# Optimization experiments

Hardware: AMD Instinct MI355X
Metric: run time of the kernel (lower is better)

Reference implementation:

```python
import jax, jax.numpy as jnp
import numpy as np

N = 50000
D_IN = 256
OUT = 16
HEADS = 32
GAT_C = OUT  # out_channels + beta_on(=0)


def _gat_conv(x, src, dst, W, att_src, att_dst, bias):
    """PyG GATConv, concat=False (mean over heads), with self-loops already appended."""
    n = x.shape[0]
    xp = (x @ W).reshape(n, HEADS, GAT_C)            # [N,H,C]
    a_s = jnp.einsum('nhc,hc->nh', xp, att_src)       # [N,H]
    a_d = jnp.einsum('nhc,hc->nh', xp, att_dst)       # [N,H]
    e = jax.nn.leaky_relu(a_s[src] + a_d[dst], 0.2)   # [E,H]
    # segment softmax over incoming edges of each dst node
    m = jax.ops.segment_max(e, dst, num_segments=n)
    e = jnp.exp(e - m[dst])
    s = jax.ops.segment_sum(e, dst, num_segments=n)
    alpha = e / (s[dst] + 1e-16)                      # [E,H]
    out = jax.ops.segment_sum(alpha[:, :, None] * xp[src], dst, num_segments=n)  # [N,H,C]
    return out.mean(axis=1) + bias                    # [N,C]


def setup_inputs() -> dict:
    key = jax.random.key(0)
    ks = jax.random.split(key, 16)
    E = 800000
    x = jax.random.normal(ks[0], (N, D_IN), dtype=jnp.float32)
    edge_index = jax.random.randint(ks[1], (2, E), 0, N, dtype=jnp.int64)
    sc = 1.0 / np.sqrt(D_IN)
    W1 = jax.random.normal(ks[2], (D_IN, HEADS * GAT_C), dtype=jnp.float32) * sc
    att_src1 = jax.random.normal(ks[3], (HEADS, GAT_C), dtype=jnp.float32) * 0.1
    att_dst1 = jax.random.normal(ks[4], (HEADS, GAT_C), dtype=jnp.float32) * 0.1
    b1 = jnp.zeros((GAT_C,), dtype=jnp.float32)
    W2 = jax.random.normal(ks[5], (D_IN, HEADS * GAT_C), dtype=jnp.float32) * sc
    att_src2 = jax.random.normal(ks[6], (HEADS, GAT_C), dtype=jnp.float32) * 0.1
    att_dst2 = jax.random.normal(ks[7], (HEADS, GAT_C), dtype=jnp.float32) * 0.1
    b2 = jnp.zeros((GAT_C,), dtype=jnp.float32)
    lin1_w = jax.random.normal(ks[8], (D_IN, 4 * OUT), dtype=jnp.float32) * sc
    lin1_b = jnp.zeros((4 * OUT,), dtype=jnp.float32)
    lin2_w = jax.random.normal(ks[9], (4 * OUT, OUT), dtype=jnp.float32) * (1.0 / np.sqrt(4 * OUT))
    lin2_b = jnp.zeros((OUT,), dtype=jnp.float32)
    return {"x": x, "edge_index": edge_index,
            "W1": W1, "att_src1": att_src1, "att_dst1": att_dst1, "b1": b1,
            "W2": W2, "att_src2": att_src2, "att_dst2": att_dst2, "b2": b2,
            "lin1_w": lin1_w, "lin1_b": lin1_b, "lin2_w": lin2_w, "lin2_b": lin2_b}


def reference(x, edge_index, W1, att_src1, att_dst1, b1, W2, att_src2, att_dst2, b2,
              lin1_w, lin1_b, lin2_w, lin2_b):
    n = x.shape[0]
    loops = jnp.arange(n, dtype=edge_index.dtype)
    # conv1: flow source_to_target on edge_index -> aggregate src=row0 into dst=row1
    src = jnp.concatenate([edge_index[0], loops])
    dst = jnp.concatenate([edge_index[1], loops])
    x_in = jax.nn.elu(_gat_conv(x, src, dst, W1, att_src1, att_dst1, b1))
    # conv2: flow target_to_source on transposed edge_index -> same effective (src,dst)
    x_out = jax.nn.elu(_gat_conv(x, src, dst, W2, att_src2, att_dst2, b2))
    x1 = jax.nn.elu(x @ lin1_w + lin1_b)
    x_self = jax.nn.elu(x1 @ lin2_w + lin2_b)
    return (x_in, x_out, x_self)
```

## Files before the change

kernel.cpp:

```cpp
#include <hip/hip_runtime.h>

typedef __bf16 bf16x8 __attribute__((ext_vector_type(8)));
typedef float  f32x4  __attribute__((ext_vector_type(4)));
typedef float  f32x2  __attribute__((ext_vector_type(2)));

#define NNODES   50000
#define DIN      256
#define HEADS    32
#define CDIM     16
#define NH       512
#define ERAW     800000
#define ZB       196
#define LDSW     280
#define LOG2E    1.4426950408889634f
#define CAST_B   12500
#define PREP_B   (CAST_B + ZB + 18)
#define GEMM_T   782
#define GEMMG    (2 * GEMM_T)
#define SCAT_B   3125
#define MLP_B    196
#define MIX1_B   (2 * SCAT_B + 3 + MLP_B)
#define MIX2_B   (2 * GEMMG + MLP_B)
#define DEGCAP   64

#if __has_builtin(__builtin_amdgcn_exp2f)
#define EXP2(x) __builtin_amdgcn_exp2f(x)
#else
#define EXP2(x) __expf((x) * 0.6931471805599453f)
#endif

__device__ __forceinline__ float b2f(unsigned short u) {
    return __uint_as_float(((unsigned)u) << 16);
}
__device__ __forceinline__ unsigned short f2b(float f) {
    unsigned v = __float_as_uint(f);
    v += 0x7fffu + ((v >> 16) & 1u);
    return (unsigned short)(v >> 16);
}

__global__ void __launch_bounds__(256) k_prep(
        const float* __restrict__ x, unsigned short* __restrict__ xb,
        const float* __restrict__ W0, const float* __restrict__ W1,
        const float* __restrict__ w1, const float* __restrict__ w2,
        unsigned short* __restrict__ Wt2, unsigned short* __restrict__ w1t,
        unsigned short* __restrict__ w2t,
        const int* __restrict__ ei, int* __restrict__ flag,
        int* __restrict__ cur) {
    __shared__ unsigned short T[64][258];
    int bid = blockIdx.x, t = threadIdx.x;

    if (bid < CAST_B) {
        int i = bid * 256 + t;
        float4 v = *(const float4*)(x + (size_t)i * 4);
        ushort4 o;
        o.x = f2b(v.x); o.y = f2b(v.y); o.z = f2b(v.z); o.w = f2b(v.w);
        *(ushort4*)(xb + (size_t)i * 4) = o;
        return;
    }
    if (bid < CAST_B + ZB) {
        int i = (bid - CAST_B) * 256 + t;
        if (i < NNODES) cur[i] = 0;
        if (bid == CAST_B && t == 0) {
            int nz = 0;
            #pragma unroll
            for (int k = 0; k < 64; ++k) nz |= ei[2 * k + 1];
            flag[0] = (nz == 0) ? 1 : 0;
        }
        return;
    }
    int tb = bid - (CAST_B + ZB);
    if (tb == 17) {
        for (int idx = t; idx < 1024; idx += 256) {
            int n = idx >> 6, k = idx & 63;
            w2t[n * 64 + k] = f2b(w2[k * CDIM + n]);
        }
        return;
    }
    const float* src; unsigned short* dst; int srcStride, doPi, tile;
    if (tb < 8)       { src = W0; dst = Wt2;             srcStride = NH; doPi = 1; tile = tb; }
    else if (tb < 16) { src = W1; dst = Wt2 + 512 * DIN; srcStride = NH; doPi = 1; tile = tb - 8; }
    else              { src = w1; dst = w1t;             srcStride = 64; doPi = 0; tile = 0; }
    int n0 = tile * 64;
    int nl = (t & 15) * 4;
    int kr = t >> 4;
    for (int kk = 0; kk < 256; kk += 16) {
        int k = kk + kr;
        float4 v = *(const float4*)(src + (size_t)k * srcStride + n0 + nl);
        T[nl + 0][k] = f2b(v.x);
        T[nl + 1][k] = f2b(v.y);
        T[nl + 2][k] = f2b(v.z);
        T[nl + 3][k] = f2b(v.w);
    }
    __syncthreads();
    int rl = t >> 2;
    int pr = doPi ? (((rl & 15) << 2) | (rl >> 4)) : rl;
    #pragma unroll
    for (int j = 0; j < 16; ++j) {
        int c4 = (t & 3) + 4 * j;
        ushort2 o0 = *(const ushort2*)&T[pr][c4 * 4];
        ushort2 o1 = *(const ushort2*)&T[pr][c4 * 4 + 2];
        ushort4 o; o.x = o0.x; o.y = o0.y; o.z = o1.x; o.w = o1.y;
        *(ushort4*)(dst + ((size_t)(n0 + rl)) * DIN + c4 * 4) = o;
    }
}

__device__ __forceinline__ void scat_body(int bid, int t,
        const int* __restrict__ ei, const int* __restrict__ flag,
        int* __restrict__ cur, int* __restrict__ csr) {
    int e = bid * 256 + t;
    int s, d;
    if (flag[0]) { s = ei[2 * e]; d = ei[2 * ERAW + 2 * e]; }
    else         { s = ei[e];     d = ei[ERAW + e]; }
    int pos = atomicAdd(&cur[d], 1);
    if (pos < DEGCAP) csr[(d << 6) + pos] = s;
}

__device__ __forceinline__ void gemm_body(int bid, int tid,
        const unsigned short* __restrict__ xb,
        const unsigned short* __restrict__ Wt,
        unsigned* __restrict__ xp8,
        const float* __restrict__ att_src, const float* __restrict__ att_dst,
        float* __restrict__ a_s, float* __restrict__ a_d,
        unsigned short* As) {
    int row0 = (bid >> 1) * 64;
    int ch   = bid & 1;
    int w = tid >> 6, lane = tid & 63;
    int r = lane & 15, quad = lane >> 4;

    {
        int row = tid >> 2, slot = tid & 3;
        const uint4* g = (const uint4*)(xb + (size_t)(row0 + row) * DIN);
        uint4* l = (uint4*)(As + row * LDSW);
        #pragma unroll
        for (int i = 0; i < 8; ++i)
            l[slot + 4 * i] = g[slot + 4 * i];
    }
    __syncthreads();

    const f32x4* As4 = (const f32x4*)att_src;
    const f32x4* Ad4 = (const f32x4*)att_dst;

    f32x4 acc[4][4] = {};
    #pragma unroll
    for (int kc = 0; kc < 8; ++kc) {
        bf16x8 a[4], b[4];
        #pragma unroll
        for (int sub = 0; sub < 4; ++sub)
            a[sub] = *(const bf16x8*)(As + (sub * 16 + r) * LDSW + kc * 32 + quad * 8);
        #pragma unroll
        for (int t = 0; t < 4; ++t) {
            int col = ch * 256 + w * 64 + t * 16 + r;
            b[t] = *(const bf16x8*)(Wt + (size_t)col * DIN + kc * 32 + quad * 8);
        }
        #pragma unroll
        for (int t = 0; t < 4; ++t)
            #pragma unroll
            for (int sub = 0; sub < 4; ++sub)
                acc[sub][t] = __builtin_amdgcn_mfma_f32_16x16x32_bf16(a[sub], b[t], acc[sub][t], 0, 0, 0);
    }
    int h = ch * 16 + w * 4 + (r >> 2);
    f32x4 sc = As4[h * 4 + (r & 3)];
    f32x4 dc = Ad4[h * 4 + (r & 3)];
    #pragma unroll
    for (int sub = 0; sub < 4; ++sub) {
        #pragma unroll
        for (int j = 0; j < 4; ++j) {
            int row = row0 + sub * 16 + quad * 4 + j;
            if (row < NNODES) {
                unsigned u = (unsigned)__builtin_amdgcn_cvt_pk_fp8_f32(
                                 acc[sub][0][j], acc[sub][1][j], 0, false);
                u = (unsigned)__builtin_amdgcn_cvt_pk_fp8_f32(
                                 acc[sub][2][j], acc[sub][3][j], (int)u, true);
                xp8[(size_t)row * 128 + ch * 64 + w * 16 + r] = u;
            }
        }
        f32x4 ps = acc[sub][0] * sc.x + acc[sub][1] * sc.y
                 + acc[sub][2] * sc.z + acc[sub][3] * sc.w;
        f32x4 pd = acc[sub][0] * dc.x + acc[sub][1] * dc.y
                 + acc[sub][2] * dc.z + acc[sub][3] * dc.w;
        #pragma unroll
        for (int m = 1; m <= 2; m <<= 1) {
            #pragma unroll
            for (int c = 0; c < 4; ++c) {
                ps[c] += __shfl_xor(ps[c], m, 64);
                pd[c] += __shfl_xor(pd[c], m, 64);
            }
        }
        int j = r & 3;
        int row = row0 + sub * 16 + quad * 4 + j;
        if (row < NNODES) {
            a_s[row * HEADS + h] = ps[j] * LOG2E;
            a_d[row * HEADS + h] = pd[j] * LOG2E;
        }
    }
}

__device__ __forceinline__ void gemm_sel(int g, int tid,
        const unsigned short* xb, const unsigned short* Wt2,
        unsigned* xp8_0, unsigned* xp8_1,
        const float* atS0, const float* atD0, const float* atS1, const float* atD1,
        float* as0, float* ad0, float* as1, float* ad1, unsigned short* SH) {
    if (g < GEMMG)
        gemm_body(g, tid, xb, Wt2, xp8_0, atS0, atD0, as0, ad0, SH);
    else
        gemm_body(g - GEMMG, tid, xb, Wt2 + 512 * DIN, xp8_1, atS1, atD1, as1, ad1, SH);
}

__device__ __forceinline__ void mlp_body(int bid, int tid,
        const unsigned short* __restrict__ xb, const unsigned short* __restrict__ w1t,
        const float* __restrict__ bb1, const unsigned short* __restrict__ w2t,
        const float* __restrict__ bb2, float* __restrict__ out,
        unsigned short* Tbase) {
    int wv = tid >> 6;
    int wave = bid * 4 + wv;
    if (wave >= GEMM_T) return;
    unsigned short* T = Tbase + wv * 64 * 72;
    int lane = tid & 63;
    int r = lane & 15, quad = lane >> 4;
    int row0 = wave * 64;

    f32x4 acc[4][4] = {};
    #pragma unroll
    for (int kc = 0; kc < 8; ++kc) {
        bf16x8 a[4];
        #pragma unroll
        for (int sub = 0; sub < 4; ++sub) {
            int row = row0 + sub * 16 + r;
            if (row0 + sub * 16 < NNODES)
                a[sub] = *(const bf16x8*)(xb + (size_t)row * DIN + kc * 32 + quad * 8);
            else {
                union { unsigned short u[8]; bf16x8 v; } z;
                #pragma unroll
                for (int j = 0; j < 8; ++j) z.u[j] = 0;
                a[sub] = z.v;
            }
        }
        #pragma unroll
        for (int t = 0; t < 4; ++t) {
            int col = t * 16 + r;
            bf16x8 b = *(const bf16x8*)(w1t + (size_t)col * DIN + kc * 32 + quad * 8);
            #pragma unroll
            for (int sub = 0; sub < 4; ++sub)
                acc[sub][t] = __builtin_amdgcn_mfma_f32_16x16x32_bf16(a[sub], b, acc[sub][t], 0, 0, 0);
        }
    }
    #pragma unroll
    for (int sub = 0; sub < 4; ++sub) {
        #pragma unroll
        for (int t = 0; t < 4; ++t) {
            int col = t * 16 + r;
            float bv = bb1[col];
            #pragma unroll
            for (int j = 0; j < 4; ++j) {
                float v = acc[sub][t][j] + bv;
                v = v > 0.f ? v : expm1f(v);
                T[(sub * 16 + quad * 4 + j) * 72 + col] = f2b(v);
            }
        }
    }
    f32x4 acc2[4] = {};
    #pragma unroll
    for (int sub = 0; sub < 4; ++sub) {
        #pragma unroll
        for (int kc = 0; kc < 2; ++kc) {
            bf16x8 a = *(const bf16x8*)&T[(sub * 16 + r) * 72 + kc * 32 + quad * 8];
            bf16x8 b = *(const bf16x8*)(w2t + r * 64 + kc * 32 + quad * 8);
            acc2[sub] = __builtin_amdgcn_mfma_f32_16x16x32_bf16(a, b, acc2[sub], 0, 0, 0);
        }
    }
    float bv2 = bb2[r];
    #pragma unroll
    for (int sub = 0; sub < 4; ++sub) {
        #pragma unroll
        for (int j = 0; j < 4; ++j) {
            int row = row0 + sub * 16 + quad * 4 + j;
            if (row < NNODES) {
                float v = acc2[sub][j] + bv2;
                out[(size_t)row * CDIM + r] = v > 0.f ? v : expm1f(v);
            }
        }
    }
}

__global__ void __launch_bounds__(256, 4) k_mix1(
        const unsigned short* __restrict__ xb, const unsigned short* __restrict__ Wt2,
        unsigned* __restrict__ xp8_0, unsigned* __restrict__ xp8_1,
        const float* __restrict__ atS0, const float* __restrict__ atD0,
        const float* __restrict__ atS1, const float* __restrict__ atD1,
        float* __restrict__ as0, float* __restrict__ ad0,
        float* __restrict__ as1, float* __restrict__ ad1,
        const int* __restrict__ ei, const int* __restrict__ flag,
        int* __restrict__ cur, int* __restrict__ csr,
        const unsigned short* __restrict__ w1t, const float* __restrict__ b1,
        const unsigned short* __restrict__ w2t, const float* __restrict__ b2,
        float* __restrict__ outm) {
    __shared__ unsigned short SH[4 * 64 * 72];
    int bid = blockIdx.x, tid = threadIdx.x;
    if (bid < 2 * SCAT_B) {
        if (bid & 1)
            gemm_sel(bid >> 1, tid, xb, Wt2, xp8_0, xp8_1, atS0, atD0, atS1, atD1,
                     as0, ad0, as1, ad1, SH);
        else
            scat_body(bid >> 1, tid, ei, flag, cur, csr);
    } else if (bid < 2 * SCAT_B + 3) {
        gemm_sel(SCAT_B + (bid - 2 * SCAT_B), tid, xb, Wt2, xp8_0, xp8_1,
                 atS0, atD0, atS1, atD1, as0, ad0, as1, ad1, SH);
    } else {
        mlp_body(bid - (2 * SCAT_B + 3), tid, xb, w1t, b1, w2t, b2, outm, SH);
    }
}

__global__ void __launch_bounds__(256, 4) k_mix2(
        const unsigned short* __restrict__ xb, const unsigned short* __restrict__ Wt2,
        unsigned* __restrict__ xp8_0, unsigned* __restrict__ xp8_1,
        const float* __restrict__ atS0, const float* __restrict__ atD0,
        const float* __restrict__ atS1, const float* __restrict__ atD1,
        float* __restrict__ as0, float* __restrict__ ad0,
        float* __restrict__ as1, float* __restrict__ ad1,
        const unsigned short* __restrict__ w1t, const float* __restrict__ b1,
        const unsigned short* __restrict__ w2t, const float* __restrict__ b2,
        float* __restrict__ outm) {
    __shared__ unsigned short SH[4 * 64 * 72];
    int bid = blockIdx.x, tid = threadIdx.x;
    if (bid < 2 * GEMMG)
        gemm_sel(bid, tid, xb, Wt2, xp8_0, xp8_1, atS0, atD0, atS1, atD1,
                 as0, ad0, as1, ad1, SH);
    else
        mlp_body(bid - 2 * GEMMG, tid, xb, w1t, b1, w2t, b2, outm, SH);
}

__global__ void k_scatter(const int* __restrict__ ei, const int* __restrict__ flag,
                          int* __restrict__ cur, int* __restrict__ csr) {
    scat_body(blockIdx.x, threadIdx.x, ei, flag, cur, csr);
}

__global__ void __launch_bounds__(256)
k_conv(const int* __restrict__ csr, const int* __restrict__ cur,
       const unsigned* __restrict__ xp8A, const float* __restrict__ asA,
       const float* __restrict__ adA, const float* __restrict__ biasA,
       float* __restrict__ outA,
       const unsigned* __restrict__ xp8B, const float* __restrict__ asB,
       const float* __restrict__ adB, const float* __restrict__ biasB,
       float* __restrict__ outB, int nsplit) {
    int bid = blockIdx.x;
    const unsigned* xp8; const float* a_s; const float* a_d;
    const float* bias; float* out; int b0;
    if (bid < nsplit) { xp8 = xp8A; a_s = asA; a_d = adA; bias = biasA; out = outA; b0 = bid; }
    else              { xp8 = xp8B; a_s = asB; a_d = adB; bias = biasB; out = outB; b0 = bid - nsplit; }
    int nd = b0 * 4 + (threadIdx.x >> 6);
    int ndu = __builtin_amdgcn_readfirstlane(nd);
    int ln = threadIdx.x & 63;
    int h  = ln >> 1;
    int cb = (ln & 1) * 8;
    float adn = a_d[nd * HEADS + h];
    int beg = ndu << 6;
    int cnt = __builtin_amdgcn_readfirstlane(cur[ndu]);
    cnt = cnt < DEGCAP ? cnt : DEGCAP;
    const uint2* xv = (const uint2*)xp8;

    float denom = 0.f;
    float acc[8] = {0, 0, 0, 0, 0, 0, 0, 0};

    #define EDGE_BODY(AV, QV, LIVE)                                        \
    {                                                                      \
        float tt = (AV) + adn;                                             \
        tt = fmaxf(tt, 0.2f * tt);                                         \
        float e = EXP2(tt);                                                \
        e = (LIVE) ? e : 0.f;                                              \
        denom += e;                                                        \
        f32x2 p0 = __builtin_amdgcn_cvt_pk_f32_fp8((int)(QV).x, false);    \
        f32x2 p1 = __builtin_amdgcn_cvt_pk_f32_fp8((int)(QV).x, true);     \
        f32x2 p2 = __builtin_amdgcn_cvt_pk_f32_fp8((int)(QV).y, false);    \
        f32x2 p3 = __builtin_amdgcn_cvt_pk_f32_fp8((int)(QV).y, true);     \
        acc[0] += e * p0.x; acc[1] += e * p0.y;                            \
        acc[2] += e * p1.x; acc[3] += e * p1.y;                            \
        acc[4] += e * p2.x; acc[5] += e * p2.y;                            \
        acc[6] += e * p3.x; acc[7] += e * p3.y;                            \
    }

    float avS = a_s[nd * HEADS + h];
    uint2 qvS = xv[(size_t)nd * 64 + ln];
    int nb = (cnt + 3) >> 2;
    float avP[4]; uint2 qvP[4]; int svN[4];
    if (nb > 0) {
        #pragma unroll
        for (int k = 0; k < 4; ++k) {
            int ce = k < cnt ? k : cnt - 1;
            int s = csr[beg + ce];
            avP[k] = a_s[s * HEADS + h];
            qvP[k] = xv[(size_t)s * 64 + ln];
        }
        #pragma unroll
        for (int k = 0; k < 4; ++k) {
            int idx = 4 + k;
            int ce = idx < cnt ? idx : cnt - 1;
            svN[k] = csr[beg + ce];
        }
    }
    __builtin_amdgcn_sched_barrier(0);
    EDGE_BODY(avS, qvS, 1)

    for (int b = 1; b < nb; ++b) {
        float avN[4]; uint2 qvN[4];
        #pragma unroll
        for (int k = 0; k < 4; ++k) {
            int s = svN[k];
            avN[k] = a_s[s * HEADS + h];
            qvN[k] = xv[(size_t)s * 64 + ln];
        }
        {
            int nbase = (b + 1 < nb ? b + 1 : nb - 1) * 4;
            #pragma unroll
            for (int k = 0; k < 4; ++k) {
                int idx = nbase + k;
                int ce = idx < cnt ? idx : cnt - 1;
                svN[k] = csr[beg + ce];
            }
        }
        __builtin_amdgcn_sched_barrier(0);
        #pragma unroll
        for (int k = 0; k < 4; ++k) EDGE_BODY(avP[k], qvP[k], 1)
        #pragma unroll
        for (int k = 0; k < 4; ++k) { avP[k] = avN[k]; qvP[k] = qvN[k]; }
    }
    if (nb > 0) {
        #pragma unroll
        for (int k = 0; k < 4; ++k) {
            int idx = (nb - 1) * 4 + k;
            EDGE_BODY(avP[k], qvP[k], idx < cnt)
        }
    }
    #undef EDGE_BODY

    float inv = 1.f / (denom + 1e-16f);
    #pragma unroll
    for (int c = 0; c < 8; ++c) acc[c] *= inv;

    #pragma unroll
    for (int mask = 2; mask <= 32; mask <<= 1) {
        #pragma unroll
        for (int c = 0; c < 8; ++c) acc[c] += __shfl_xor(acc[c], mask, 64);
    }
    if (ln < 2) {
        #pragma unroll
        for (int c2 = 0; c2 < 8; ++c2) {
            int c = cb + c2;
            float o = acc[c2] * (1.0f / HEADS) + bias[c];
            out[(size_t)nd * CDIM + c] = o > 0.f ? o : expm1f(o);
        }
    }
}

extern "C" void kernel_launch(void* const* d_in, const int* in_sizes, int n_in,
                              void* d_out, int out_size, void* d_ws, size_t ws_size,
                              hipStream_t stream) {
    const float* x  = (const float*)d_in[0];
    const int* ei   = (const int*)d_in[1];
    const float* W[2]    = {(const float*)d_in[2], (const float*)d_in[6]};
    const float* atS[2]  = {(const float*)d_in[3], (const float*)d_in[7]};
    const float* atD[2]  = {(const float*)d_in[4], (const float*)d_in[8]};
    const float* bias[2] = {(const float*)d_in[5], (const float*)d_in[9]};
    const float* w1 = (const float*)d_in[10];
    const float* b1 = (const float*)d_in[11];
    const float* w2 = (const float*)d_in[12];
    const float* b2 = (const float*)d_in[13];
    float* out = (float*)d_out;
    char* ws = (char*)d_ws;

    unsigned* xp8_0 = (unsigned*)(ws);
    unsigned* xp8_1 = (unsigned*)(ws + 25600000);
    unsigned short* xb  = (unsigned short*)(ws + 51200000);
    unsigned short* Wt2 = (unsigned short*)(ws + 76800000);
    unsigned short* w1t = (unsigned short*)(ws + 77324288);
    unsigned short* w2t = (unsigned short*)(ws + 77357056);
    float* as0 = (float*)(ws + 77359104);
    float* ad0 = (float*)(ws + 83759104);
    float* as1 = (float*)(ws + 90159104);
    float* ad1 = (float*)(ws + 96559104);
    int* cur   = (int*)(ws + 102959104);
    int* flag  = (int*)(ws + 103159104);

    const size_t NEED_T1 = 115959168;
    if (ws_size >= NEED_T1) {
        int* csr = (int*)(ws + 103159168);
        k_prep<<<PREP_B, 256, 0, stream>>>(x, xb, W[0], W[1], w1, w2,
                                           Wt2, w1t, w2t, ei, flag, cur);
        k_mix1<<<MIX1_B, 256, 0, stream>>>(xb, Wt2, xp8_0, xp8_1,
                                           atS[0], atD[0], atS[1], atD[1],
                                           as0, ad0, as1, ad1,
                                           ei, flag, cur, csr,
                                           w1t, b1, w2t, b2, out + 1600000);
        k_conv<<<25000, 256, 0, stream>>>(csr, cur,
                                          xp8_0, as0, ad0, bias[0], out,
                                          xp8_1, as1, ad1, bias[1], out + 800000,
                                          12500);
    } else {
        int* csr = (int*)(ws + 51200000);
        k_prep   <<<PREP_B, 256, 0, stream>>>(x, xb, W[0], W[1], w1, w2,
                                              Wt2, w1t, w2t, ei, flag, cur);
        k_mix2   <<<MIX2_B, 256, 0, stream>>>(xb, Wt2, xp8_0, xp8_1,
                                              atS[0], atD[0], atS[1], atD[1],
                                              as0, ad0, as1, ad1,
                                              w1t, b1, w2t, b2, out + 1600000);
        k_scatter<<<SCAT_B, 256, 0, stream>>>(ei, flag, cur, csr);
        k_conv   <<<25000, 256, 0, stream>>>(csr, cur,
                                             xp8_0, as0, ad0, bias[0], out,
                                             xp8_1, as1, ad1, bias[1], out + 800000,
                                             12500);
    }
}
```

Measured before the change: 401.3 us.

## Fuse both GAT GEMMs per block, move MLP into conv tail kernel

The GEMM block now computes both convolution projections from a single LDS-staged tile of x, so the x tile is loaded once instead of twice. The MLP branch moves out of the mix kernel and into a combined tail kernel with the edge aggregation, and each MLP block now handles 64 rows with one wave per 16 output columns. The aim is better reuse of x and better overlap of the light MLP work with the gather-heavy conv. In exchange there are fewer, longer GEMM blocks, which weakens interleaving with scatter. The fallback path's csr offset also changes, which could overlap other workspace regions.

```diff
diff --git a/kernel.cpp b/kernel.cpp
--- a/kernel.cpp
+++ b/kernel.cpp
@@ -16,11 +16,11 @@
 #define CAST_B   12500
 #define PREP_B   (CAST_B + ZB + 18)
 #define GEMM_T   782
-#define GEMMG    (2 * GEMM_T)
+#define GEMM2_B  (2 * GEMM_T)
 #define SCAT_B   3125
-#define MLP_B    196
-#define MIX1_B   (2 * SCAT_B + 3 + MLP_B)
-#define MIX2_B   (2 * GEMMG + MLP_B)
+#define MLP_B    782
+#define MIX1_B   (2 * GEMM2_B + (SCAT_B - GEMM2_B))
+#define TAIL_B   (MLP_B + 25000)
 #define DEGCAP   64
 
 #if __has_builtin(__builtin_amdgcn_exp2f)
@@ -115,12 +115,14 @@
     if (pos < DEGCAP) csr[(d << 6) + pos] = s;
 }
 
-__device__ __forceinline__ void gemm_body(int bid, int tid,
+__device__ __forceinline__ void gemm2_body(int bid, int tid,
         const unsigned short* __restrict__ xb,
-        const unsigned short* __restrict__ Wt,
-        unsigned* __restrict__ xp8,
-        const float* __restrict__ att_src, const float* __restrict__ att_dst,
-        float* __restrict__ a_s, float* __restrict__ a_d,
+        const unsigned short* __restrict__ Wt2,
+        unsigned* __restrict__ xp8_0, unsigned* __restrict__ xp8_1,
+        const float* __restrict__ atS0, const float* __restrict__ atD0,
+        const float* __restrict__ atS1, const float* __restrict__ atD1,
+        float* __restrict__ as0, float* __restrict__ ad0,
+        float* __restrict__ as1, float* __restrict__ ad1,
         unsigned short* As) {
     int row0 = (bid >> 1) * 64;
     int ch   = bid & 1;
@@ -137,219 +139,146 @@
     }
     __syncthreads();
 
-    const f32x4* As4 = (const f32x4*)att_src;
-    const f32x4* Ad4 = (const f32x4*)att_dst;
-
-    f32x4 acc[4][4] = {};
-    #pragma unroll
-    for (int kc = 0; kc < 8; ++kc) {
-        bf16x8 a[4], b[4];
-        #pragma unroll
-        for (int sub = 0; sub < 4; ++sub)
-            a[sub] = *(const bf16x8*)(As + (sub * 16 + r) * LDSW + kc * 32 + quad * 8);
-        #pragma unroll
-        for (int t = 0; t < 4; ++t) {
-            int col = ch * 256 + w * 64 + t * 16 + r;
-            b[t] = *(const bf16x8*)(Wt + (size_t)col * DIN + kc * 32 + quad * 8);
-        }
-        #pragma unroll
-        for (int t = 0; t < 4; ++t)
+    int h = ch * 16 + w * 4 + (r >> 2);
+
+    for (int cv = 0; cv < 2; ++cv) {
+        const unsigned short* Wt = Wt2 + (size_t)cv * 512 * DIN;
+        unsigned* xp8 = cv ? xp8_1 : xp8_0;
+        const f32x4* As4 = (const f32x4*)(cv ? atS1 : atS0);
+        const f32x4* Ad4 = (const f32x4*)(cv ? atD1 : atD0);
+        float* a_s = cv ? as1 : as0;
+        float* a_d = cv ? ad1 : ad0;
+
+        f32x4 acc[4][4] = {};
+        #pragma unroll
+        for (int kc = 0; kc < 8; ++kc) {
+            bf16x8 a[4], b[4];
             #pragma unroll
             for (int sub = 0; sub < 4; ++sub)
-                acc[sub][t] = __builtin_amdgcn_mfma_f32_16x16x32_bf16(a[sub], b[t], acc[sub][t], 0, 0, 0);
-    }
-    int h = ch * 16 + w * 4 + (r >> 2);
-    f32x4 sc = As4[h * 4 + (r & 3)];
-    f32x4 dc = Ad4[h * 4 + (r & 3)];
-    #pragma unroll
-    for (int sub = 0; sub < 4; ++sub) {
-        #pragma unroll
-        for (int j = 0; j < 4; ++j) {
+                a[sub] = *(const bf16x8*)(As + (sub * 16 + r) * LDSW + kc * 32 + quad * 8);
+            #pragma unroll
+            for (int t = 0; t < 4; ++t) {
+                int col = ch * 256 + w * 64 + t * 16 + r;
+                b[t] = *(const bf16x8*)(Wt + (size_t)col * DIN + kc * 32 + quad * 8);
+            }
+            #pragma unroll
+            for (int t = 0; t < 4; ++t)
+                #pragma unroll
+                for (int sub = 0; sub < 4; ++sub)
+                    acc[sub][t] = __builtin_amdgcn_mfma_f32_16x16x32_bf16(a[sub], b[t], acc[sub][t], 0, 0, 0);
+        }
+        f32x4 sc = As4[h * 4 + (r & 3)];
+        f32x4 dc = Ad4[h * 4 + (r & 3)];
+        #pragma unroll
+        for (int sub = 0; sub < 4; ++sub) {
+            #pragma unroll
+            for (int j = 0; j < 4; ++j) {
+                int row = row0 + sub * 16 + quad * 4 + j;
+                if (row < NNODES) {
+                    unsigned u = (unsigned)__builtin_amdgcn_cvt_pk_fp8_f32(
+                                     acc[sub][0][j], acc[sub][1][j], 0, false);
+                    u = (unsigned)__builtin_amdgcn_cvt_pk_fp8_f32(
+                                     acc[sub][2][j], acc[sub][3][j], (int)u, true);
+                    xp8[(size_t)row * 128 + ch * 64 + w * 16 + r] = u;
+                }
+            }
+            f32x4 ps = acc[sub][0] * sc.x + acc[sub][1] * sc.y
+                     + acc[sub][2] * sc.z + acc[sub][3] * sc.w;
+            f32x4 pd = acc[sub][0] * dc.x + acc[sub][1] * dc.y
+                     + acc[sub][2] * dc.z + acc[sub][3] * dc.w;
+            #pragma unroll
+            for (int m = 1; m <= 2; m <<= 1) {
+                #pragma unroll
+                for (int c = 0; c < 4; ++c) {
+                    ps[c] += __shfl_xor(ps[c], m, 64);
+                    pd[c] += __shfl_xor(pd[c], m, 64);
+                }
+            }
+            int j = r & 3;
             int row = row0 + sub * 16 + quad * 4 + j;
             if (row < NNODES) {
-                unsigned u = (unsigned)__builtin_amdgcn_cvt_pk_fp8_f32(
-                                 acc[sub][0][j], acc[sub][1][j], 0, false);
-                u = (unsigned)__builtin_amdgcn_cvt_pk_fp8_f32(
-                                 acc[sub][2][j], acc[sub][3][j], (int)u, true);
-                xp8[(size_t)row * 128 + ch * 64 + w * 16 + r] = u;
-            }
-        }
-        f32x4 ps = acc[sub][0] * sc.x + acc[sub][1] * sc.y
-                 + acc[sub][2] * sc.z + acc[sub][3] * sc.w;
-        f32x4 pd = acc[sub][0] * dc.x + acc[sub][1] * dc.y
-                 + acc[sub][2] * dc.z + acc[sub][3] * dc.w;
-        #pragma unroll
-        for (int m = 1; m <= 2; m <<= 1) {
-            #pragma unroll
-            for (int c = 0; c < 4; ++c) {
-                ps[c] += __shfl_xor(ps[c], m, 64);
-                pd[c] += __shfl_xor(pd[c], m, 64);
-            }
-        }
-        int j = r & 3;
-        int row = row0 + sub * 16 + quad * 4 + j;
-        if (row < NNODES) {
-            a_s[row * HEADS + h] = ps[j] * LOG2E;
-            a_d[row * HEADS + h] = pd[j] * LOG2E;
-        }
-    }
-}
-
-__device__ __forceinline__ void gemm_sel(int g, int tid,
-        const unsigned short* xb, const unsigned short* Wt2,
-        unsigned* xp8_0, unsigned* xp8_1,
-        const float* atS0, const float* atD0, const float* atS1, const float* atD1,
-        float* as0, float* ad0, float* as1, float* ad1, unsigned short* SH) {
-    if (g < GEMMG)
-        gemm_body(g, tid, xb, Wt2, xp8_0, atS0, atD0, as0, ad0, SH);
-    else
-        gemm_body(g - GEMMG, tid, xb, Wt2 + 512 * DIN, xp8_1, atS1, atD1, as1, ad1, SH);
+                a_s[row * HEADS + h] = ps[j] * LOG2E;
+                a_d[row * HEADS + h] = pd[j] * LOG2E;
+            }
+        }
+    }
 }
 
 __device__ __forceinline__ void mlp_body(int bid, int tid,
         const unsigned short* __restrict__ xb, const unsigned short* __restrict__ w1t,
         const float* __restrict__ bb1, const unsigned short* __restrict__ w2t,
         const float* __restrict__ bb2, float* __restrict__ out,
-        unsigned short* Tbase) {
-    int wv = tid >> 6;
-    int wave = bid * 4 + wv;
-    if (wave >= GEMM_T) return;
-    unsigned short* T = Tbase + wv * 64 * 72;
-    int lane = tid & 63;
+        unsigned short* T) {
+    int w = tid >> 6, lane = tid & 63;
     int r = lane & 15, quad = lane >> 4;
-    int row0 = wave * 64;
-
-    f32x4 acc[4][4] = {};
+    int row0 = bid * 64;
+
+    f32x4 acc[4] = {};
     #pragma unroll
     for (int kc = 0; kc < 8; ++kc) {
-        bf16x8 a[4];
+        bf16x8 b = *(const bf16x8*)(w1t + (size_t)(w * 16 + r) * DIN + kc * 32 + quad * 8);
         #pragma unroll
         for (int sub = 0; sub < 4; ++sub) {
+            bf16x8 a;
             int row = row0 + sub * 16 + r;
             if (row0 + sub * 16 < NNODES)
-                a[sub] = *(const bf16x8*)(xb + (size_t)row * DIN + kc * 32 + quad * 8);
+                a = *(const bf16x8*)(xb + (size_t)row * DIN + kc * 32 + quad * 8);
             else {
                 union { unsigned short u[8]; bf16x8 v; } z;
                 #pragma unroll
                 for (int j = 0; j < 8; ++j) z.u[j] = 0;
-                a[sub] = z.v;
-            }
-        }
-        #pragma unroll
-        for (int t = 0; t < 4; ++t) {
-            int col = t * 16 + r;
-            bf16x8 b = *(const bf16x8*)(w1t + (size_t)col * DIN + kc * 32 + quad * 8);
-            #pragma unroll
-            for (int sub = 0; sub < 4; ++sub)
-                acc[sub][t] = __builtin_amdgcn_mfma_f32_16x16x32_bf16(a[sub], b, acc[sub][t], 0, 0, 0);
-        }
-    }
-    #pragma unroll
-    for (int sub = 0; sub < 4; ++sub) {
-        #pragma unroll
-        for (int t = 0; t < 4; ++t) {
-            int col = t * 16 + r;
-            float bv = bb1[col];
+                a = z.v;
+            }
+            acc[sub] = __builtin_amdgcn_mfma_f32_16x16x32_bf16(a, b, acc[sub], 0, 0, 0);
+        }
+    }
+    {
+        int col = w * 16 + r;
+        float bv = bb1[col];
+        #pragma unroll
+        for (int sub = 0; sub < 4; ++sub) {
             #pragma unroll
             for (int j = 0; j < 4; ++j) {
-                float v = acc[sub][t][j] + bv;
+                float v = acc[sub][j] + bv;
                 v = v > 0.f ? v : expm1f(v);
                 T[(sub * 16 + quad * 4 + j) * 72 + col] = f2b(v);
             }
         }
     }
-    f32x4 acc2[4] = {};
-    #pragma unroll
-    for (int sub = 0; sub < 4; ++sub) {
-        #pragma unroll
-        for (int kc = 0; kc < 2; ++kc) {
-            bf16x8 a = *(const bf16x8*)&T[(sub * 16 + r) * 72 + kc * 32 + quad * 8];
-            bf16x8 b = *(const bf16x8*)(w2t + r * 64 + kc * 32 + quad * 8);
-            acc2[sub] = __builtin_amdgcn_mfma_f32_16x16x32_bf16(a, b, acc2[sub], 0, 0, 0);
-        }
+    __syncthreads();
+    f32x4 acc2 = {};
+    #pragma unroll
+    for (int kc = 0; kc < 2; ++kc) {
+        bf16x8 a = *(const bf16x8*)&T[(w * 16 + r) * 72 + kc * 32 + quad * 8];
+        bf16x8 b = *(const bf16x8*)(w2t + r * 64 + kc * 32 + quad * 8);
+        acc2 = __builtin_amdgcn_mfma_f32_16x16x32_bf16(a, b, acc2, 0, 0, 0);
     }
     float bv2 = bb2[r];
     #pragma unroll
-    for (int sub = 0; sub < 4; ++sub) {
-        #pragma unroll
-        for (int j = 0; j < 4; ++j) {
-            int row = row0 + sub * 16 + quad * 4 + j;
-            if (row < NNODES) {
-                float v = acc2[sub][j] + bv2;
-                out[(size_t)row * CDIM + r] = v > 0.f ? v : expm1f(v);
-            }
-        }
-    }
-}
-
-__global__ void __launch_bounds__(256, 4) k_mix1(
-        const unsigned short* __restrict__ xb, const unsigned short* __restrict__ Wt2,
-        unsigned* __restrict__ xp8_0, unsigned* __restrict__ xp8_1,
-        const float* __restrict__ atS0, const float* __restrict__ atD0,
-        const float* __restrict__ atS1, const float* __restrict__ atD1,
-        float* __restrict__ as0, float* __restrict__ ad0,
-        float* __restrict__ as1, float* __restrict__ ad1,
-        const int* __restrict__ ei, const int* __restrict__ flag,
-        int* __restrict__ cur, int* __restrict__ csr,
-        const unsigned short* __restrict__ w1t, const float* __restrict__ b1,
-        const unsigned short* __restrict__ w2t, const float* __restrict__ b2,
-        float* __restrict__ outm) {
-    __shared__ unsigned short SH[4 * 64 * 72];
-    int bid = blockIdx.x, tid = threadIdx.x;
-    if (bid < 2 * SCAT_B) {
-        if (bid & 1)
-            gemm_sel(bid >> 1, tid, xb, Wt2, xp8_0, xp8_1, atS0, atD0, atS1, atD1,
-                     as0, ad0, as1, ad1, SH);
-        else
-            scat_body(bid >> 1, tid, ei, flag, cur, csr);
-    } else if (bid < 2 * SCAT_B + 3) {
-        gemm_sel(SCAT_B + (bid - 2 * SCAT_B), tid, xb, Wt2, xp8_0, xp8_1,
-                 atS0, atD0, atS1, atD1, as0, ad0, as1, ad1, SH);
-    } else {
-        mlp_body(bid - (2 * SCAT_B + 3), tid, xb, w1t, b1, w2t, b2, outm, SH);
-    }
-}
-
-__global__ void __launch_bounds__(256, 4) k_mix2(
-        const unsigned short* __restrict__ xb, const unsigned short* __restrict__ Wt2,
-        unsigned* __restrict__ xp8_0, unsigned* __restrict__ xp8_1,
-        const float* __restrict__ atS0, const float* __restrict__ atD0,
-        const float* __restrict__ atS1, const float* __restrict__ atD1,
-        float* __restrict__ as0, float* __restrict__ ad0,
-        float* __restrict__ as1, float* __restrict__ ad1,
-        const unsigned short* __restrict__ w1t, const float* __restrict__ b1,
-        const unsigned short* __restrict__ w2t, const float* __restrict__ b2,
-        float* __restrict__ outm) {
-    __shared__ unsigned short SH[4 * 64 * 72];
-    int bid = blockIdx.x, tid = threadIdx.x;
-    if (bid < 2 * GEMMG)
-        gemm_sel(bid, tid, xb, Wt2, xp8_0, xp8_1, atS0, atD0, atS1, atD1,
-                 as0, ad0, as1, ad1, SH);
-    else
-        mlp_body(bid - 2 * GEMMG, tid, xb, w1t, b1, w2t, b2, outm, SH);
-}
-
-__global__ void k_scatter(const int* __restrict__ ei, const int* __restrict__ flag,
-                          int* __restrict__ cur, int* __restrict__ csr) {
-    scat_body(blockIdx.x, threadIdx.x, ei, flag, cur, csr);
-}
-
-__global__ void __launch_bounds__(256)
-k_conv(const int* __restrict__ csr, const int* __restrict__ cur,
-       const unsigned* __restrict__ xp8A, const float* __restrict__ asA,
-       const float* __restrict__ adA, const float* __restrict__ biasA,
-       float* __restrict__ outA,
-       const unsigned* __restrict__ xp8B, const float* __restrict__ asB,
-       const float* __restrict__ adB, const float* __restrict__ biasB,
-       float* __restrict__ outB, int nsplit) {
-    int bid = blockIdx.x;
+    for (int j = 0; j < 4; ++j) {
+        int row = row0 + w * 16 + quad * 4 + j;
+        if (row < NNODES) {
+            float v = acc2[j] + bv2;
+            out[(size_t)row * CDIM + r] = v > 0.f ? v : expm1f(v);
+        }
+    }
+}
+
+__device__ __forceinline__ void conv_body(int cbid, int tid,
+        const int* __restrict__ csr, const int* __restrict__ cur,
+        const unsigned* __restrict__ xp8A, const float* __restrict__ asA,
+        const float* __restrict__ adA, const float* __restrict__ biasA,
+        float* __restrict__ outA,
+        const unsigned* __restrict__ xp8B, const float* __restrict__ asB,
+        const float* __restrict__ adB, const float* __restrict__ biasB,
+        float* __restrict__ outB, int nsplit) {
     const unsigned* xp8; const float* a_s; const float* a_d;
     const float* bias; float* out; int b0;
-    if (bid < nsplit) { xp8 = xp8A; a_s = asA; a_d = adA; bias = biasA; out = outA; b0 = bid; }
-    else              { xp8 = xp8B; a_s = asB; a_d = adB; bias = biasB; out = outB; b0 = bid - nsplit; }
-    int nd = b0 * 4 + (threadIdx.x >> 6);
+    if (cbid < nsplit) { xp8 = xp8A; a_s = asA; a_d = adA; bias = biasA; out = outA; b0 = cbid; }
+    else               { xp8 = xp8B; a_s = asB; a_d = adB; bias = biasB; out = outB; b0 = cbid - nsplit; }
+    int nd = b0 * 4 + (tid >> 6);
     int ndu = __builtin_amdgcn_readfirstlane(nd);
-    int ln = threadIdx.x & 63;
+    int ln = tid & 63;
     int h  = ln >> 1;
     int cb = (ln & 1) * 8;
     float adn = a_d[nd * HEADS + h];
@@ -451,6 +380,66 @@
     }
 }
 
+__global__ void __launch_bounds__(256, 4) k_mix1(
+        const unsigned short* __restrict__ xb, const unsigned short* __restrict__ Wt2,
+        unsigned* __restrict__ xp8_0, unsigned* __restrict__ xp8_1,
+        const float* __restrict__ atS0, const float* __restrict__ atD0,
+        const float* __restrict__ atS1, const float* __restrict__ atD1,
+        float* __restrict__ as0, float* __restrict__ ad0,
+        float* __restrict__ as1, float* __restrict__ ad1,
+        const int* __restrict__ ei, const int* __restrict__ flag,
+        int* __restrict__ cur, int* __restrict__ csr) {
+    __shared__ unsigned short As[64 * LDSW];
+    int bid = blockIdx.x, tid = threadIdx.x;
+    if (bid < 2 * GEMM2_B) {
+        if (bid & 1)
+            gemm2_body(bid >> 1, tid, xb, Wt2, xp8_0, xp8_1,
+                       atS0, atD0, atS1, atD1, as0, ad0, as1, ad1, As);
+        else
+            scat_body(bid >> 1, tid, ei, flag, cur, csr);
+    } else {
+        scat_body(GEMM2_B + (bid - 2 * GEMM2_B), tid, ei, flag, cur, csr);
+    }
+}
+
+__global__ void __launch_bounds__(256, 4) k_mix2(
+        const unsigned short* __restrict__ xb, const unsigned short* __restrict__ Wt2,
+        unsigned* __restrict__ xp8_0, unsigned* __restrict__ xp8_1,
+        const float* __restrict__ atS0, const float* __restrict__ atD0,
+        const float* __restrict__ atS1, const float* __restrict__ atD1,
+        float* __restrict__ as0, float* __restrict__ ad0,
+        float* __restrict__ as1, float* __restrict__ ad1) {
+    __shared__ unsigned short As[64 * LDSW];
+    gemm2_body(blockIdx.x, threadIdx.x, xb, Wt2, xp8_0, xp8_1,
+               atS0, atD0, atS1, atD1, as0, ad0, as1, ad1, As);
+}
+
+__global__ void k_scatter(const int* __restrict__ ei, const int* __restrict__ flag,
+                          int* __restrict__ cur, int* __restrict__ csr) {
+    scat_body(blockIdx.x, threadIdx.x, ei, flag, cur, csr);
+}
+
+__global__ void __launch_bounds__(256, 8) k_tail(
+        const unsigned short* __restrict__ xb, const unsigned short* __restrict__ w1t,
+        const float* __restrict__ b1, const unsigned short* __restrict__ w2t,
+        const float* __restrict__ b2, float* __restrict__ outm,
+        const int* __restrict__ csr, const int* __restrict__ cur,
+        const unsigned* __restrict__ xp8A, const float* __restrict__ asA,
+        const float* __restrict__ adA, const float* __restrict__ biasA,
+        float* __restrict__ outA,
+        const unsigned* __restrict__ xp8B, const float* __restrict__ asB,
+        const float* __restrict__ adB, const float* __restrict__ biasB,
+        float* __restrict__ outB) {
+    __shared__ unsigned short T[64 * 72];
+    int bid = blockIdx.x, tid = threadIdx.x;
+    if (bid < MLP_B)
+        mlp_body(bid, tid, xb, w1t, b1, w2t, b2, outm, T);
+    else
+        conv_body(bid - MLP_B, tid, csr, cur,
+                  xp8A, asA, adA, biasA, outA,
+                  xp8B, asB, adB, biasB, outB, 12500);
+}
+
 extern "C" void kernel_launch(void* const* d_in, const int* in_sizes, int n_in,
                               void* d_out, int out_size, void* d_ws, size_t ws_size,
                               hipStream_t stream) {
@@ -488,24 +477,22 @@
         k_mix1<<<MIX1_B, 256, 0, stream>>>(xb, Wt2, xp8_0, xp8_1,
                                            atS[0], atD[0], atS[1], atD[1],
                                            as0, ad0, as1, ad1,
-                                           ei, flag, cur, csr,
-                                           w1t, b1, w2t, b2, out + 1600000);
-        k_conv<<<25000, 256, 0, stream>>>(csr, cur,
-                                          xp8_0, as0, ad0, bias[0], out,
-                                          xp8_1, as1, ad1, bias[1], out + 800000,
-                                          12500);
+                                           ei, flag, cur, csr);
+        k_tail<<<TAIL_B, 256, 0, stream>>>(xb, w1t, b1, w2t, b2, out + 1600000,
+                                           csr, cur,
+                                           xp8_0, as0, ad0, bias[0], out,
+                                           xp8_1, as1, ad1, bias[1], out + 800000);
     } else {
-        int* csr = (int*)(ws + 51200000);
+        int* csr = (int*)(ws + 103159168);
         k_prep   <<<PREP_B, 256, 0, stream>>>(x, xb, W[0], W[1], w1, w2,
                                               Wt2, w1t, w2t, ei, flag, cur);
-        k_mix2   <<<MIX2_B, 256, 0, stream>>>(xb, Wt2, xp8_0, xp8_1,
-                                              atS[0], atD[0], atS[1], atD[1],
-                                              as0, ad0, as1, ad1,
-                                              w1t, b1, w2t, b2, out + 1600000);
+        k_mix2   <<<GEMM2_B, 256, 0, stream>>>(xb, Wt2, xp8_0, xp8_1,
+                                               atS[0], atD[0], atS[1], atD[1],
+                                               as0, ad0, as1, ad1);
         k_scatter<<<SCAT_B, 256, 0, stream>>>(ei, flag, cur, csr);
-        k_conv   <<<25000, 256, 0, stream>>>(csr, cur,
-                                             xp8_0, as0, ad0, bias[0], out,
-                                             xp8_1, as1, ad1, bias[1], out + 800000,
-                                             12500);
-    }
-}
+        k_tail   <<<TAIL_B, 256, 0, stream>>>(xb, w1t, b1, w2t, b2, out + 1600000,
+                                              csr, cur,
+                                              xp8_0, as0, ad0, bias[0], out,
+                                              xp8_1, as1, ad1, bias[1], out + 800000);
+    }
+}
```

After: 621.3 us. 1.55x slower.

## Split fused mix kernel into GEMM and aux kernels, prefetch B fragments

Applied to the files above, without the earlier changes.

The projection GEMM moves out of the interleaved mixed kernel into its own k_gemms launch with a dedicated 64-row LDS tile and launch bounds of 3 waves per SIMD. Scatter and the MLP go to a separate k_aux kernel, or to k_mlp and k_scatter on the fallback path. Inside the GEMM loop the weight fragments for the next k-chunk are now loaded before the current MFMAs, with a sched_barrier, to hide global latency. The cost is an extra launch and the loss of overlap between the atomic-heavy scatter and the compute-bound GEMM.

```diff
diff --git a/kernel.cpp b/kernel.cpp
--- a/kernel.cpp
+++ b/kernel.cpp
@@ -19,8 +19,7 @@
 #define GEMMG    (2 * GEMM_T)
 #define SCAT_B   3125
 #define MLP_B    196
-#define MIX1_B   (2 * SCAT_B + 3 + MLP_B)
-#define MIX2_B   (2 * GEMMG + MLP_B)
+#define AUX_B    (SCAT_B + MLP_B)
 #define DEGCAP   64
 
 #if __has_builtin(__builtin_amdgcn_exp2f)
@@ -137,28 +136,39 @@
     }
     __syncthreads();
 
+    const unsigned short* Bb = Wt + (size_t)(ch * 256 + w * 64 + r) * DIN + quad * 8;
+
+    f32x4 acc[4][4] = {};
+    bf16x8 bP[4];
+    #pragma unroll
+    for (int t = 0; t < 4; ++t)
+        bP[t] = *(const bf16x8*)(Bb + (size_t)t * 16 * DIN);
+
+    #pragma unroll
+    for (int kc = 0; kc < 8; ++kc) {
+        bf16x8 bN[4];
+        if (kc < 7) {
+            #pragma unroll
+            for (int t = 0; t < 4; ++t)
+                bN[t] = *(const bf16x8*)(Bb + (size_t)t * 16 * DIN + (kc + 1) * 32);
+        }
+        bf16x8 a[4];
+        #pragma unroll
+        for (int sub = 0; sub < 4; ++sub)
+            a[sub] = *(const bf16x8*)(As + (sub * 16 + r) * LDSW + kc * 32 + quad * 8);
+        __builtin_amdgcn_sched_barrier(0);
+        #pragma unroll
+        for (int t = 0; t < 4; ++t)
+            #pragma unroll
+            for (int sub = 0; sub < 4; ++sub)
+                acc[sub][t] = __builtin_amdgcn_mfma_f32_16x16x32_bf16(a[sub], bP[t], acc[sub][t], 0, 0, 0);
+        #pragma unroll
+        for (int t = 0; t < 4; ++t) bP[t] = bN[t];
+    }
+
+    int h = ch * 16 + w * 4 + (r >> 2);
     const f32x4* As4 = (const f32x4*)att_src;
     const f32x4* Ad4 = (const f32x4*)att_dst;
-
-    f32x4 acc[4][4] = {};
-    #pragma unroll
-    for (int kc = 0; kc < 8; ++kc) {
-        bf16x8 a[4], b[4];
-        #pragma unroll
-        for (int sub = 0; sub < 4; ++sub)
-            a[sub] = *(const bf16x8*)(As + (sub * 16 + r) * LDSW + kc * 32 + quad * 8);
-        #pragma unroll
-        for (int t = 0; t < 4; ++t) {
-            int col = ch * 256 + w * 64 + t * 16 + r;
-            b[t] = *(const bf16x8*)(Wt + (size_t)col * DIN + kc * 32 + quad * 8);
-        }
-        #pragma unroll
-        for (int t = 0; t < 4; ++t)
-            #pragma unroll
-            for (int sub = 0; sub < 4; ++sub)
-                acc[sub][t] = __builtin_amdgcn_mfma_f32_16x16x32_bf16(a[sub], b[t], acc[sub][t], 0, 0, 0);
-    }
-    int h = ch * 16 + w * 4 + (r >> 2);
     f32x4 sc = As4[h * 4 + (r & 3)];
     f32x4 dc = Ad4[h * 4 + (r & 3)];
     #pragma unroll
@@ -193,17 +203,6 @@
             a_d[row * HEADS + h] = pd[j] * LOG2E;
         }
     }
-}
-
-__device__ __forceinline__ void gemm_sel(int g, int tid,
-        const unsigned short* xb, const unsigned short* Wt2,
-        unsigned* xp8_0, unsigned* xp8_1,
-        const float* atS0, const float* atD0, const float* atS1, const float* atD1,
-        float* as0, float* ad0, float* as1, float* ad1, unsigned short* SH) {
-    if (g < GEMMG)
-        gemm_body(g, tid, xb, Wt2, xp8_0, atS0, atD0, as0, ad0, SH);
-    else
-        gemm_body(g - GEMMG, tid, xb, Wt2 + 512 * DIN, xp8_1, atS1, atD1, as1, ad1, SH);
 }
 
 __device__ __forceinline__ void mlp_body(int bid, int tid,
@@ -282,56 +281,46 @@
     }
 }
 
-__global__ void __launch_bounds__(256, 4) k_mix1(
+__global__ void __launch_bounds__(256, 3) k_gemms(
         const unsigned short* __restrict__ xb, const unsigned short* __restrict__ Wt2,
         unsigned* __restrict__ xp8_0, unsigned* __restrict__ xp8_1,
         const float* __restrict__ atS0, const float* __restrict__ atD0,
         const float* __restrict__ atS1, const float* __restrict__ atD1,
         float* __restrict__ as0, float* __restrict__ ad0,
-        float* __restrict__ as1, float* __restrict__ ad1,
+        float* __restrict__ as1, float* __restrict__ ad1) {
+    __shared__ unsigned short As[64 * LDSW];
+    int bid = blockIdx.x, tid = threadIdx.x;
+    if (bid < GEMMG)
+        gemm_body(bid, tid, xb, Wt2, xp8_0, atS0, atD0, as0, ad0, As);
+    else
+        gemm_body(bid - GEMMG, tid, xb, Wt2 + 512 * DIN, xp8_1, atS1, atD1, as1, ad1, As);
+}
+
+__global__ void __launch_bounds__(256, 4) k_aux(
         const int* __restrict__ ei, const int* __restrict__ flag,
         int* __restrict__ cur, int* __restrict__ csr,
-        const unsigned short* __restrict__ w1t, const float* __restrict__ b1,
-        const unsigned short* __restrict__ w2t, const float* __restrict__ b2,
-        float* __restrict__ outm) {
+        const unsigned short* __restrict__ xb, const unsigned short* __restrict__ w1t,
+        const float* __restrict__ b1, const unsigned short* __restrict__ w2t,
+        const float* __restrict__ b2, float* __restrict__ outm) {
     __shared__ unsigned short SH[4 * 64 * 72];
     int bid = blockIdx.x, tid = threadIdx.x;
-    if (bid < 2 * SCAT_B) {
-        if (bid & 1)
-            gemm_sel(bid >> 1, tid, xb, Wt2, xp8_0, xp8_1, atS0, atD0, atS1, atD1,
-                     as0, ad0, as1, ad1, SH);
-        else
-            scat_body(bid >> 1, tid, ei, flag, cur, csr);
-    } else if (bid < 2 * SCAT_B + 3) {
-        gemm_sel(SCAT_B + (bid - 2 * SCAT_B), tid, xb, Wt2, xp8_0, xp8_1,
-                 atS0, atD0, atS1, atD1, as0, ad0, as1, ad1, SH);
-    } else {
-        mlp_body(bid - (2 * SCAT_B + 3), tid, xb, w1t, b1, w2t, b2, outm, SH);
-    }
-}
-
-__global__ void __launch_bounds__(256, 4) k_mix2(
-        const unsigned short* __restrict__ xb, const unsigned short* __restrict__ Wt2,
-        unsigned* __restrict__ xp8_0, unsigned* __restrict__ xp8_1,
-        const float* __restrict__ atS0, const float* __restrict__ atD0,
-        const float* __restrict__ atS1, const float* __restrict__ atD1,
-        float* __restrict__ as0, float* __restrict__ ad0,
-        float* __restrict__ as1, float* __restrict__ ad1,
-        const unsigned short* __restrict__ w1t, const float* __restrict__ b1,
-        const unsigned short* __restrict__ w2t, const float* __restrict__ b2,
-        float* __restrict__ outm) {
-    __shared__ unsigned short SH[4 * 64 * 72];
-    int bid = blockIdx.x, tid = threadIdx.x;
-    if (bid < 2 * GEMMG)
-        gemm_sel(bid, tid, xb, Wt2, xp8_0, xp8_1, atS0, atD0, atS1, atD1,
-                 as0, ad0, as1, ad1, SH);
+    if (bid < SCAT_B)
+        scat_body(bid, tid, ei, flag, cur, csr);
     else
-        mlp_body(bid - 2 * GEMMG, tid, xb, w1t, b1, w2t, b2, outm, SH);
+        mlp_body(bid - SCAT_B, tid, xb, w1t, b1, w2t, b2, outm, SH);
 }
 
 __global__ void k_scatter(const int* __restrict__ ei, const int* __restrict__ flag,
                           int* __restrict__ cur, int* __restrict__ csr) {
     scat_body(blockIdx.x, threadIdx.x, ei, flag, cur, csr);
+}
+
+__global__ void __launch_bounds__(256, 4)
+k_mlp(const unsigned short* __restrict__ xb, const unsigned short* __restrict__ w1t,
+      const float* __restrict__ b1, const unsigned short* __restrict__ w2t,
+      const float* __restrict__ b2, float* __restrict__ outm) {
+    __shared__ unsigned short SH[4 * 64 * 72];
+    mlp_body(blockIdx.x, threadIdx.x, xb, w1t, b1, w2t, b2, outm, SH);
 }
 
 __global__ void __launch_bounds__(256)
@@ -483,25 +472,25 @@
     const size_t NEED_T1 = 115959168;
     if (ws_size >= NEED_T1) {
         int* csr = (int*)(ws + 103159168);
-        k_prep<<<PREP_B, 256, 0, stream>>>(x, xb, W[0], W[1], w1, w2,
-                                           Wt2, w1t, w2t, ei, flag, cur);
-        k_mix1<<<MIX1_B, 256, 0, stream>>>(xb, Wt2, xp8_0, xp8_1,
-                                           atS[0], atD[0], atS[1], atD[1],
-                                           as0, ad0, as1, ad1,
-                                           ei, flag, cur, csr,
-                                           w1t, b1, w2t, b2, out + 1600000);
-        k_conv<<<25000, 256, 0, stream>>>(csr, cur,
-                                          xp8_0, as0, ad0, bias[0], out,
-                                          xp8_1, as1, ad1, bias[1], out + 800000,
-                                          12500);
+        k_prep <<<PREP_B, 256, 0, stream>>>(x, xb, W[0], W[1], w1, w2,
+                                            Wt2, w1t, w2t, ei, flag, cur);
+        k_gemms<<<2 * GEMMG, 256, 0, stream>>>(xb, Wt2, xp8_0, xp8_1,
+                                               atS[0], atD[0], atS[1], atD[1],
+                                               as0, ad0, as1, ad1);
+        k_aux  <<<AUX_B, 256, 0, stream>>>(ei, flag, cur, csr,
+                                           xb, w1t, b1, w2t, b2, out + 1600000);
+        k_conv <<<25000, 256, 0, stream>>>(csr, cur,
+                                           xp8_0, as0, ad0, bias[0], out,
+                                           xp8_1, as1, ad1, bias[1], out + 800000,
+                                           12500);
     } else {
         int* csr = (int*)(ws + 51200000);
         k_prep   <<<PREP_B, 256, 0, stream>>>(x, xb, W[0], W[1], w1, w2,
                                               Wt2, w1t, w2t, ei, flag, cur);
-        k_mix2   <<<MIX2_B, 256, 0, stream>>>(xb, Wt2, xp8_0, xp8_1,
-                                              atS[0], atD[0], atS[1], atD[1],
-                                              as0, ad0, as1, ad1,
-                                              w1t, b1, w2t, b2, out + 1600000);
+        k_gemms  <<<2 * GEMMG, 256, 0, stream>>>(xb, Wt2, xp8_0, xp8_1,
+                                                 atS[0], atD[0], atS[1], atD[1],
+                                                 as0, ad0, as1, ad1);
+        k_mlp    <<<MLP_B, 256, 0, stream>>>(xb, w1t, b1, w2t, b2, out + 1600000);
         k_scatter<<<SCAT_B, 256, 0, stream>>>(ei, flag, cur, csr);
         k_conv   <<<25000, 256, 0, stream>>>(csr, cur,
                                              xp8_0, as0, ad0, bias[0], out,
```

After: 417.3 us. 1.04x slower.
